# Kernel optimization log

Hardware: AMD Instinct MI355X
Metric: run time of the kernel (lower is better)

The kernel has to match this reference:

```python
import jax, jax.numpy as jnp
import numpy as np

SEQ_LEN = 12          # seq_length
K = 8                 # nsamples = 2 * num_samples
RADII = (4.0 + 1e-06, 8.0 + 1e-06, 12.0 + 1e-06)
COUT = (64, 128, 256)


def _group(xyz, s_xyz, radius):
    # ball query via knn + radius mask: xyz (B,N,3) queries, s_xyz (B,M,3) keys
    d2 = jnp.sum((xyz[:, :, None, :] - s_xyz[:, None, :, :]) ** 2, axis=-1)  # (B,N,M)
    neg, idx = jax.lax.top_k(-d2, K)                                          # (B,N,K)
    valid = (-neg) <= radius * radius
    # points outside the ball are replaced by the nearest neighbor (pad-with-first)
    return jnp.where(valid, idx, idx[..., :1])


def _gather(a, idx):
    # a (B,M,C), idx (B,N,K) -> (B,N,K,C)
    return jax.vmap(lambda t, i: t[i])(a, idx)


def _cell(xyz, feat, state, W, b, radius, cout):
    # PointRNN cell: group state points around current points, fuse
    # [displacement, current feature, state feature] with a shared linear,
    # then max-pool over the K neighbors. New state xyz = current xyz.
    B, N, _ = xyz.shape
    if state is None:
        s_xyz, s_feat = xyz, jnp.zeros((B, N, cout), xyz.dtype)
    else:
        s_xyz, s_feat = state
    idx = _group(xyz, s_xyz, radius)
    n_xyz = _gather(s_xyz, idx)                      # (B,N,K,3)
    n_feat = _gather(s_feat, idx)                    # (B,N,K,cout)
    disp = n_xyz - xyz[:, :, None, :]
    parts = [disp]
    if feat is not None:
        cin = feat.shape[-1]
        parts.append(jnp.broadcast_to(feat[:, :, None, :], (B, N, K, cin)))
    parts.append(n_feat)
    h = jnp.concatenate(parts, axis=-1) @ W + b      # (B,N,K,cout)
    return (xyz, jnp.max(h, axis=2))                 # (xyz, (B,N,cout))


def _forward(frames, W1, b1, W2, b2, W3, b3, Wm, bm, Wl, bl):
    half = SEQ_LEN // 2
    s1 = s2 = s3 = None
    # encode
    for i in range(half):
        s1 = _cell(frames[:, i], None, s1, W1, b1, RADII[0], COUT[0])
        s2 = _cell(s1[0], s1[1], s2, W2, b2, RADII[1], COUT[1])
        s3 = _cell(s2[0], s2[1], s3, W3, b3, RADII[2], COUT[2])
    # decode
    input_frame = frames[:, half - 1]
    preds = []
    for i in range(half, SEQ_LEN):
        s1 = _cell(input_frame, None, s1, W1, b1, RADII[0], COUT[0])
        s2 = _cell(s1[0], s1[1], s2, W2, b2, RADII[1], COUT[1])
        s3 = _cell(s2[0], s2[1], s3, W3, b3, RADII[2], COUT[2])
        h = jax.nn.relu(s3[1] @ Wm + bm)             # MLP([256,64]) = Lin+ReLU
        motion = h @ Wl + bl                         # (B,N,3)
        input_frame = input_frame + motion
        preds.append(input_frame)
    return jnp.stack(preds, axis=1)                  # (B, T/2, N, 3)


def setup_inputs() -> dict:
    key = jax.random.key(0)
    ks = jax.random.split(key, 12)
    B, N = 16, 512
    frames = jax.random.normal(ks[0], (B, SEQ_LEN, N, 3), jnp.float32) * 2.0

    def lin(k, fin, fout):
        k1, k2 = jax.random.split(k)
        s = 1.0 / np.sqrt(fin)
        return (jax.random.uniform(k1, (fin, fout), jnp.float32, -s, s),
                jax.random.uniform(k2, (fout,), jnp.float32, -s, s))

    W1, b1 = lin(ks[1], 3 + 0 + 64, 64)
    W2, b2 = lin(ks[2], 3 + 64 + 128, 128)
    W3, b3 = lin(ks[3], 3 + 128 + 256, 256)
    Wm, bm = lin(ks[4], 256, 64)
    Wl, bl = lin(ks[5], 64, 3)
    return {"frames": frames, "W1": W1, "b1": b1, "W2": W2, "b2": b2,
            "W3": W3, "b3": b3, "Wm": Wm, "bm": bm, "Wl": Wl, "bl": bl}


def reference(frames, W1, b1, W2, b2, W3, b3, Wm, bm, Wl, bl):
    return _forward(frames, W1, b1, W2, b2, W3, b3, Wm, bm, Wl, bl)
```

## Files before the change

kernel.cpp:

```cpp
#include <hip/hip_runtime.h>
#include <math.h>

#define BB 16
#define NN 512
#define KNN 8
#define SEQ 12
#define TQ 8
#define QB 32
#define PB 16

typedef __attribute__((ext_vector_type(8))) short bf8_t;
typedef __attribute__((ext_vector_type(4))) float f4_t;

__device__ __forceinline__ ushort f2b(float x) {
    uint u = __float_as_uint(x);
    return (ushort)((u + 0x7fffu + ((u >> 16) & 1u)) >> 16);
}
__device__ __forceinline__ float b2f(ushort h) {
    return __uint_as_float((uint)h << 16);
}
__device__ __forceinline__ void cvt8(const float* __restrict__ p,
                                     bf8_t& h, bf8_t& l) {
    float4 x0 = *(const float4*)p;
    float4 x1 = *(const float4*)(p + 4);
    float v[8] = {x0.x, x0.y, x0.z, x0.w, x1.x, x1.y, x1.z, x1.w};
#pragma unroll
    for (int i = 0; i < 8; ++i) {
        ushort hh = f2b(v[i]);
        h[i] = (short)hh;
        l[i] = (short)f2b(v[i] - b2f(hh));
    }
}

__device__ __forceinline__ void knn_body(
        const float* __restrict__ xqp, int xq_bs,
        const float* __restrict__ xsp, int xs_bs,
        int* __restrict__ idx1, int* __restrict__ idx2, int* __restrict__ idx3,
        float r2a, float r2b, float r2c,
        int ntile, int b, float* __restrict__ sm) {
    float* s   = sm;
    float* cdp = sm + 1544;
    int*   cip = (int*)(sm + 1544 + 2304);
    const int tid = threadIdx.x;

    for (int j = tid; j < NN; j += 256) {
        const float* p = xsp + (long)b * xs_bs + j * 3;
        int o = 3 * j + (j >> 6);
        s[o + 0] = p[0]; s[o + 1] = p[1]; s[o + 2] = p[2];
    }
    __syncthreads();

    int qi  = tid / TQ;
    int sub = tid % TQ;
    int n = ntile * QB + qi;
    const float* q = xqp + (long)b * xq_bs + n * 3;
    float qx = q[0], qy = q[1], qz2 = q[2];

    float bd[KNN];
    int   bi[KNN];
#pragma unroll
    for (int k = 0; k < KNN; ++k) { bd[k] = 1e30f; bi[k] = 0; }

    int j0 = sub * (NN / TQ);
    int sbase = 3 * j0 + sub;
#pragma unroll 4
    for (int jj = 0; jj < NN / TQ; ++jj) {
        float dx = s[sbase + 3 * jj + 0] - qx;
        float dy = s[sbase + 3 * jj + 1] - qy;
        float dz = s[sbase + 3 * jj + 2] - qz2;
        float d2 = fmaf(dx, dx, fmaf(dy, dy, dz * dz));
        if (d2 < bd[KNN - 1]) {
            bd[KNN - 1] = d2; bi[KNN - 1] = j0 + jj;
#pragma unroll
            for (int k = KNN - 1; k >= 1; --k) {
                if (bd[k] < bd[k - 1]) {
                    float td = bd[k]; bd[k] = bd[k - 1]; bd[k - 1] = td;
                    int   ti = bi[k]; bi[k] = bi[k - 1]; bi[k - 1] = ti;
                }
            }
        }
    }

    float* cdq = cdp + (qi * TQ + sub) * (KNN + 1);
    int*   ciq = cip + (qi * TQ + sub) * (KNN + 1);
#pragma unroll
    for (int k = 0; k < KNN; ++k) { cdq[k] = bd[k]; ciq[k] = bi[k]; }
    cdq[KNN] = 1e30f; ciq[KNN] = 0x7fffffff;
    __syncthreads();

    for (int stride = TQ / 2; stride >= 1; stride >>= 1) {
        if (sub < stride) {
            float* ca = cdp + (qi * TQ + sub) * (KNN + 1);
            float* cb = cdp + (qi * TQ + sub + stride) * (KNN + 1);
            int*   ja_p = cip + (qi * TQ + sub) * (KNN + 1);
            int*   jb_p = cip + (qi * TQ + sub + stride) * (KNN + 1);
            float rd[KNN]; int ri[KNN];
            int ia = 0, ib = 0;
#pragma unroll
            for (int k = 0; k < KNN; ++k) {
                float da = ca[ia], db = cb[ib];
                int   ja = ja_p[ia], jb = jb_p[ib];
                bool ta = (da < db) || (da == db && ja < jb);
                rd[k] = ta ? da : db; ri[k] = ta ? ja : jb;
                ia += ta ? 1 : 0; ib += ta ? 0 : 1;
            }
#pragma unroll
            for (int k = 0; k < KNN; ++k) { ca[k] = rd[k]; ja_p[k] = ri[k]; }
        }
        __syncthreads();
    }

    if (sub == 0) {
        long base = ((long)(b * NN + n)) * KNN;
        float* c0  = cdp + qi * TQ * (KNN + 1);
        int*   j0p = cip + qi * TQ * (KNN + 1);
        int i0 = j0p[0];
#pragma unroll
        for (int k = 0; k < KNN; ++k) {
            float d = c0[k]; int j = j0p[k];
            idx1[base + k] = (d <= r2a) ? j : i0;
            idx2[base + k] = (d <= r2b) ? j : i0;
            idx3[base + k] = (d <= r2c) ? j : i0;
        }
    }
}

__global__ __launch_bounds__(256) void init_kernel(
        const float* __restrict__ frames, int FB,
        int* __restrict__ i1, int* __restrict__ i2, int* __restrict__ i3,
        float r2a, float r2b, float r2c,
        const float* __restrict__ W1, const float* __restrict__ W2,
        const float* __restrict__ W3, const float* __restrict__ Wm,
        ushort* __restrict__ w1h, ushort* __restrict__ w1l,
        ushort* __restrict__ w2h, ushort* __restrict__ w2l,
        ushort* __restrict__ w3h, ushort* __restrict__ w3l,
        ushort* __restrict__ w2fh, ushort* __restrict__ w2fl,
        ushort* __restrict__ w3fh, ushort* __restrict__ w3fl,
        ushort* __restrict__ wmh, ushort* __restrict__ wml) {
    __shared__ float sm[1544 + 2304 + 2304];
    int bx = blockIdx.x;
    if (bx < 256) {
        int xcd = bx & 7, slot = bx >> 3;
        int b = xcd * 2 + (slot & 1), ntile = slot >> 1;
        knn_body(frames, FB, frames, FB, i1, i2, i3, r2a, r2b, r2c,
                 ntile, b, sm);
        return;
    }
    int t = (bx - 256) * 256 + threadIdx.x;
    float v; ushort* ph; ushort* pl; int idx;
    if (t < 4096)        { int n = t >> 6, k = t & 63;
        v = W1[(3 + k) * 64 + n];   ph = w1h;  pl = w1l;  idx = t; }
    else if (t < 20480)  { int u = t - 4096, n = u >> 7, k = u & 127;
        v = W2[(67 + k) * 128 + n]; ph = w2h;  pl = w2l;  idx = u; }
    else if (t < 86016)  { int u = t - 20480, n = u >> 8, k = u & 255;
        v = W3[(131 + k) * 256 + n]; ph = w3h; pl = w3l;  idx = u; }
    else if (t < 94208)  { int u = t - 86016, n = u >> 6, k = u & 63;
        v = W2[(3 + k) * 128 + n];  ph = w2fh; pl = w2fl; idx = u; }
    else if (t < 126976) { int u = t - 94208, n = u >> 7, k = u & 127;
        v = W3[(3 + k) * 256 + n];  ph = w3fh; pl = w3fl; idx = u; }
    else if (t < 143360) { int u = t - 126976, n = u >> 8, k = u & 255;
        v = Wm[k * 64 + n];         ph = wmh;  pl = wml;  idx = u; }
    else return;
    ushort h = f2b(v);
    ph[idx] = h; pl[idx] = f2b(v - b2f(h));
}

template<bool FIRST>
__global__ __launch_bounds__(512, 4) void cells_kernel(
        const float* __restrict__ xq, int xq_bs,
        const float* __restrict__ xs, int xs_bs,
        const int* __restrict__ i1, const int* __restrict__ i2,
        const int* __restrict__ i3,
        const float* __restrict__ G1p, const float* __restrict__ G2p,
        const float* __restrict__ G3p,
        ushort* __restrict__ s1h, ushort* __restrict__ s1l,
        ushort* __restrict__ s2h, ushort* __restrict__ s2l,
        ushort* __restrict__ s3h, ushort* __restrict__ s3l,
        const float* __restrict__ W1, const float* __restrict__ b1,
        const float* __restrict__ W2, const float* __restrict__ b2,
        const float* __restrict__ W3, const float* __restrict__ b3,
        const ushort* __restrict__ w2fh, const ushort* __restrict__ w2fl,
        const ushort* __restrict__ w3fh, const ushort* __restrict__ w3fl,
        const ushort* __restrict__ wmh, const ushort* __restrict__ wml,
        const float* __restrict__ bm,
        const float* __restrict__ Wl, const float* __restrict__ bl,
        float* __restrict__ xnext, int xn_bs, int do_head) {
    __shared__ float s1s[PB][68];
    __shared__ float s2s[PB][132];
    __shared__ float s3b[PB][260];
    __shared__ float hs[PB][64];
    __shared__ float dsp[3][PB][KNN][3];
    __shared__ int   jss[3][PB][KNN];

    const int tid = threadIdx.x;
    const int blk = blockIdx.x;
    const int xcd = blk & 7, slot = blk >> 3;
    const int b   = xcd * 2 + (slot >> 5);
    const int n0  = (slot & 31) << 4;
    const long row0 = (long)b * NN + n0;
    const long bN = (long)b * NN;
    const int wv = tid >> 6, lane = tid & 63;
    const int fm = lane & 15, quad = lane >> 4;

    for (int t = tid; t < 3 * PB * KNN; t += 512) {
        int r = t >> 7, rem = t & 127, p = rem >> 3, k = rem & 7;
        const int* ix = (r == 0) ? i1 : ((r == 1) ? i2 : i3);
        int j = ix[(row0 + p) * KNN + k];
        jss[r][p][k] = j;
        const float* sp = xs + (long)b * xs_bs + j * 3;
        const float* qp = xq + (long)b * xq_bs + (n0 + p) * 3;
        dsp[r][p][k][0] = sp[0] - qp[0];
        dsp[r][p][k][1] = sp[1] - qp[1];
        dsp[r][p][k][2] = sp[2] - qp[2];
    }
    __syncthreads();

    {
        int co = tid & 63, q = tid >> 6;
        float g1r[2][KNN];
        if (!FIRST) {
#pragma unroll
            for (int r = 0; r < 2; ++r)
#pragma unroll
                for (int k = 0; k < KNN; ++k)
                    g1r[r][k] = G1p[(bN + jss[0][2 * q + r][k]) * 64 + co];
        }
        float wx = W1[co], wy = W1[64 + co], wz = W1[128 + co];
        float bz = b1[co];
#pragma unroll
        for (int r = 0; r < 2; ++r) {
            int p = 2 * q + r;
            float acc = -1e30f;
#pragma unroll
            for (int k = 0; k < KNN; ++k) {
                float v = fmaf(dsp[0][p][k][0], wx, bz);
                v = fmaf(dsp[0][p][k][1], wy, v);
                v = fmaf(dsp[0][p][k][2], wz, v);
                if (!FIRST) v += g1r[r][k];
                acc = fmaxf(acc, v);
            }
            s1s[p][co] = acc;
            ushort h = f2b(acc);
            s1h[(row0 + p) * 64 + co] = h;
            s1l[(row0 + p) * 64 + co] = f2b(acc - b2f(h));
        }
    }
    __syncthreads();

    float4 g2r[KNN];
    {
        int c4 = tid & 31, g = tid >> 5;
        if (!FIRST) {
#pragma unroll
            for (int k = 0; k < KNN; ++k)
                g2r[k] = ((const float4*)G2p)[(bN + jss[1][g][k]) * 32 + c4];
        }
    }

    {
        int col = wv * 16 + fm;
        float bz = b2[col];
        f4_t acc = {bz, bz, bz, bz};
#pragma unroll
        for (int k0 = 0; k0 < 64; k0 += 32) {
            bf8_t ah, al; cvt8(&s1s[fm][k0 + quad * 8], ah, al);
            bf8_t bh = *(const bf8_t*)(w2fh + col * 64 + k0 + quad * 8);
            bf8_t bl = *(const bf8_t*)(w2fl + col * 64 + k0 + quad * 8);
            acc = __builtin_amdgcn_mfma_f32_16x16x32_bf16(ah, bh, acc, 0, 0, 0);
            acc = __builtin_amdgcn_mfma_f32_16x16x32_bf16(ah, bl, acc, 0, 0, 0);
            acc = __builtin_amdgcn_mfma_f32_16x16x32_bf16(al, bh, acc, 0, 0, 0);
        }
#pragma unroll
        for (int r = 0; r < 4; ++r) s2s[quad * 4 + r][col] = acc[r];
    }
    __syncthreads();

    {
        int c4 = tid & 31, g = tid >> 5;
        float4 bse = *(float4*)&s2s[g][c4 * 4];
        float4 wx = ((const float4*)W2)[c4];
        float4 wy = ((const float4*)(W2 + 128))[c4];
        float4 wz = ((const float4*)(W2 + 256))[c4];
        float4 m = make_float4(-1e30f, -1e30f, -1e30f, -1e30f);
#pragma unroll
        for (int k = 0; k < KNN; ++k) {
            float dx = dsp[1][g][k][0], dy = dsp[1][g][k][1], dz = dsp[1][g][k][2];
            float4 v;
            v.x = fmaf(dz, wz.x, fmaf(dy, wy.x, fmaf(dx, wx.x, bse.x)));
            v.y = fmaf(dz, wz.y, fmaf(dy, wy.y, fmaf(dx, wx.y, bse.y)));
            v.z = fmaf(dz, wz.z, fmaf(dy, wy.z, fmaf(dx, wx.z, bse.z)));
            v.w = fmaf(dz, wz.w, fmaf(dy, wy.w, fmaf(dx, wx.w, bse.w)));
            if (!FIRST) {
                v.x += g2r[k].x; v.y += g2r[k].y;
                v.z += g2r[k].z; v.w += g2r[k].w;
            }
            m.x = fmaxf(m.x, v.x); m.y = fmaxf(m.y, v.y);
            m.z = fmaxf(m.z, v.z); m.w = fmaxf(m.w, v.w);
        }
        *(float4*)&s2s[g][c4 * 4] = m;
        ushort4 mh, ml;
        mh.x = f2b(m.x); ml.x = f2b(m.x - b2f(mh.x));
        mh.y = f2b(m.y); ml.y = f2b(m.y - b2f(mh.y));
        mh.z = f2b(m.z); ml.z = f2b(m.z - b2f(mh.z));
        mh.w = f2b(m.w); ml.w = f2b(m.w - b2f(mh.w));
        *(ushort4*)&s2h[(row0 + g) * 128 + c4 * 4] = mh;
        *(ushort4*)&s2l[(row0 + g) * 128 + c4 * 4] = ml;
    }
    __syncthreads();

    float4 g3r[2][KNN];
    {
        int c4 = tid & 63, g = tid >> 6;
        if (!FIRST) {
#pragma unroll
            for (int r = 0; r < 2; ++r)
#pragma unroll
                for (int k = 0; k < KNN; ++k)
                    g3r[r][k] = ((const float4*)G3p)[(bN + jss[2][2 * g + r][k]) * 64 + c4];
        }
    }

    {
        int col0 = wv * 16 + fm, col1 = (wv + 8) * 16 + fm;
        float bz0 = b3[col0], bz1 = b3[col1];
        f4_t a0 = {bz0, bz0, bz0, bz0};
        f4_t a1 = {bz1, bz1, bz1, bz1};
#pragma unroll
        for (int k0 = 0; k0 < 128; k0 += 32) {
            bf8_t ah, al; cvt8(&s2s[fm][k0 + quad * 8], ah, al);
            bf8_t b0h = *(const bf8_t*)(w3fh + col0 * 128 + k0 + quad * 8);
            bf8_t b0l = *(const bf8_t*)(w3fl + col0 * 128 + k0 + quad * 8);
            bf8_t b1h = *(const bf8_t*)(w3fh + col1 * 128 + k0 + quad * 8);
            bf8_t b1l = *(const bf8_t*)(w3fl + col1 * 128 + k0 + quad * 8);
            a0 = __builtin_amdgcn_mfma_f32_16x16x32_bf16(ah, b0h, a0, 0, 0, 0);
            a0 = __builtin_amdgcn_mfma_f32_16x16x32_bf16(ah, b0l, a0, 0, 0, 0);
            a0 = __builtin_amdgcn_mfma_f32_16x16x32_bf16(al, b0h, a0, 0, 0, 0);
            a1 = __builtin_amdgcn_mfma_f32_16x16x32_bf16(ah, b1h, a1, 0, 0, 0);
            a1 = __builtin_amdgcn_mfma_f32_16x16x32_bf16(ah, b1l, a1, 0, 0, 0);
            a1 = __builtin_amdgcn_mfma_f32_16x16x32_bf16(al, b1h, a1, 0, 0, 0);
        }
#pragma unroll
        for (int r = 0; r < 4; ++r) {
            s3b[quad * 4 + r][col0] = a0[r];
            s3b[quad * 4 + r][col1] = a1[r];
        }
    }
    __syncthreads();

    {
        int c4 = tid & 63, g = tid >> 6;
        float4 wx = ((const float4*)W3)[c4];
        float4 wy = ((const float4*)(W3 + 256))[c4];
        float4 wz = ((const float4*)(W3 + 512))[c4];
#pragma unroll
        for (int r = 0; r < 2; ++r) {
            int p = 2 * g + r;
            float4 bse = *(float4*)&s3b[p][c4 * 4];
            float4 m = make_float4(-1e30f, -1e30f, -1e30f, -1e30f);
#pragma unroll
            for (int k = 0; k < KNN; ++k) {
                float dx = dsp[2][p][k][0], dy = dsp[2][p][k][1], dz = dsp[2][p][k][2];
                float4 v;
                v.x = fmaf(dz, wz.x, fmaf(dy, wy.x, fmaf(dx, wx.x, bse.x)));
                v.y = fmaf(dz, wz.y, fmaf(dy, wy.y, fmaf(dx, wx.y, bse.y)));
                v.z = fmaf(dz, wz.z, fmaf(dy, wy.z, fmaf(dx, wx.z, bse.z)));
                v.w = fmaf(dz, wz.w, fmaf(dy, wy.w, fmaf(dx, wx.w, bse.w)));
                if (!FIRST) {
                    v.x += g3r[r][k].x; v.y += g3r[r][k].y;
                    v.z += g3r[r][k].z; v.w += g3r[r][k].w;
                }
                m.x = fmaxf(m.x, v.x); m.y = fmaxf(m.y, v.y);
                m.z = fmaxf(m.z, v.z); m.w = fmaxf(m.w, v.w);
            }
            *(float4*)&s3b[p][c4 * 4] = m;
            ushort4 mh, ml;
            mh.x = f2b(m.x); ml.x = f2b(m.x - b2f(mh.x));
            mh.y = f2b(m.y); ml.y = f2b(m.y - b2f(mh.y));
            mh.z = f2b(m.z); ml.z = f2b(m.z - b2f(mh.z));
            mh.w = f2b(m.w); ml.w = f2b(m.w - b2f(mh.w));
            *(ushort4*)&s3h[(row0 + p) * 256 + c4 * 4] = mh;
            *(ushort4*)&s3l[(row0 + p) * 256 + c4 * 4] = ml;
        }
    }

    if (do_head) {
        __syncthreads();
        if (wv < 4) {
            int col = wv * 16 + fm;
            float bz = bm[col];
            f4_t acc = {bz, bz, bz, bz};
#pragma unroll
            for (int k0 = 0; k0 < 256; k0 += 32) {
                bf8_t ah, al; cvt8(&s3b[fm][k0 + quad * 8], ah, al);
                bf8_t bh = *(const bf8_t*)(wmh + col * 256 + k0 + quad * 8);
                bf8_t bl = *(const bf8_t*)(wml + col * 256 + k0 + quad * 8);
                acc = __builtin_amdgcn_mfma_f32_16x16x32_bf16(ah, bh, acc, 0, 0, 0);
                acc = __builtin_amdgcn_mfma_f32_16x16x32_bf16(ah, bl, acc, 0, 0, 0);
                acc = __builtin_amdgcn_mfma_f32_16x16x32_bf16(al, bh, acc, 0, 0, 0);
            }
#pragma unroll
            for (int r = 0; r < 4; ++r)
                hs[quad * 4 + r][col] = fmaxf(acc[r], 0.f);
        }
        __syncthreads();
        if (tid < PB * 3) {
            int p = tid / 3, d = tid % 3;
            float m = bl[d];
#pragma unroll 4
            for (int c = 0; c < 64; ++c)
                m = fmaf(hs[p][c], Wl[c * 3 + d], m);
            const float* qp = xq + (long)b * xq_bs + (n0 + p) * 3;
            xnext[(long)b * xn_bs + (n0 + p) * 3 + d] = qp[d] + m;
        }
    }
}

template<int N>
__device__ __forceinline__ void gemmTile(
        const ushort* __restrict__ Ah, const ushort* __restrict__ Al,
        const ushort* __restrict__ Bh, const ushort* __restrict__ Bl,
        float* __restrict__ G, int rb, int cb, int tid, ushort* lds) {
    const int row0 = rb * 128, c0 = cb * 64;
    ushort* ah = lds;
    ushort* al = lds + 128 * 40;
    ushort* bh = lds + 256 * 40;
    ushort* bl = lds + 320 * 40;
    const int wv = tid >> 6, lane = tid & 63;
    const int m = lane & 15, quad = lane >> 4;
    const int wm0 = wv * 32;
    const int lr = tid >> 2, ls = (tid & 3) * 8;

    f4_t acc[2][4];
#pragma unroll
    for (int rt = 0; rt < 2; ++rt)
#pragma unroll
        for (int ct = 0; ct < 4; ++ct) acc[rt][ct] = (f4_t){0.f, 0.f, 0.f, 0.f};

    bf8_t pah0, pah1, pal0, pal1, pbh, pbl;
    pah0 = *(const bf8_t*)(Ah + (long)(row0 + lr) * N + ls);
    pah1 = *(const bf8_t*)(Ah + (long)(row0 + 64 + lr) * N + ls);
    pal0 = *(const bf8_t*)(Al + (long)(row0 + lr) * N + ls);
    pal1 = *(const bf8_t*)(Al + (long)(row0 + 64 + lr) * N + ls);
    pbh  = *(const bf8_t*)(Bh + (long)(c0 + lr) * N + ls);
    pbl  = *(const bf8_t*)(Bl + (long)(c0 + lr) * N + ls);

    for (int k0 = 0; k0 < N; k0 += 32) {
        if (k0) __syncthreads();
        *(bf8_t*)(ah + lr * 40 + ls) = pah0;
        *(bf8_t*)(ah + (64 + lr) * 40 + ls) = pah1;
        *(bf8_t*)(al + lr * 40 + ls) = pal0;
        *(bf8_t*)(al + (64 + lr) * 40 + ls) = pal1;
        *(bf8_t*)(bh + lr * 40 + ls) = pbh;
        *(bf8_t*)(bl + lr * 40 + ls) = pbl;
        __syncthreads();
        if (k0 + 32 < N) {
            int kn = k0 + 32;
            pah0 = *(const bf8_t*)(Ah + (long)(row0 + lr) * N + kn + ls);
            pah1 = *(const bf8_t*)(Ah + (long)(row0 + 64 + lr) * N + kn + ls);
            pal0 = *(const bf8_t*)(Al + (long)(row0 + lr) * N + kn + ls);
            pal1 = *(const bf8_t*)(Al + (long)(row0 + 64 + lr) * N + kn + ls);
            pbh  = *(const bf8_t*)(Bh + (long)(c0 + lr) * N + kn + ls);
            pbl  = *(const bf8_t*)(Bl + (long)(c0 + lr) * N + kn + ls);
        }
        bf8_t a0h = *(const bf8_t*)(ah + (wm0 + m) * 40 + quad * 8);
        bf8_t a0l = *(const bf8_t*)(al + (wm0 + m) * 40 + quad * 8);
        bf8_t a1h = *(const bf8_t*)(ah + (wm0 + 16 + m) * 40 + quad * 8);
        bf8_t a1l = *(const bf8_t*)(al + (wm0 + 16 + m) * 40 + quad * 8);
#pragma unroll
        for (int ct = 0; ct < 4; ++ct) {
            bf8_t bth = *(const bf8_t*)(bh + (ct * 16 + m) * 40 + quad * 8);
            bf8_t btl = *(const bf8_t*)(bl + (ct * 16 + m) * 40 + quad * 8);
            acc[0][ct] = __builtin_amdgcn_mfma_f32_16x16x32_bf16(a0h, bth, acc[0][ct], 0, 0, 0);
            acc[0][ct] = __builtin_amdgcn_mfma_f32_16x16x32_bf16(a0h, btl, acc[0][ct], 0, 0, 0);
            acc[0][ct] = __builtin_amdgcn_mfma_f32_16x16x32_bf16(a0l, bth, acc[0][ct], 0, 0, 0);
            acc[1][ct] = __builtin_amdgcn_mfma_f32_16x16x32_bf16(a1h, bth, acc[1][ct], 0, 0, 0);
            acc[1][ct] = __builtin_amdgcn_mfma_f32_16x16x32_bf16(a1h, btl, acc[1][ct], 0, 0, 0);
            acc[1][ct] = __builtin_amdgcn_mfma_f32_16x16x32_bf16(a1l, bth, acc[1][ct], 0, 0, 0);
        }
    }
#pragma unroll
    for (int rt = 0; rt < 2; ++rt)
#pragma unroll
        for (int ct = 0; ct < 4; ++ct) {
            int col = c0 + ct * 16 + m;
#pragma unroll
            for (int r = 0; r < 4; ++r)
                G[(long)(row0 + wm0 + rt * 16 + quad * 4 + r) * N + col] = acc[rt][ct][r];
        }
}

__global__ __launch_bounds__(256) void gemmG_kernel(
        const ushort* __restrict__ s1h, const ushort* __restrict__ s1l,
        const ushort* __restrict__ s2h, const ushort* __restrict__ s2l,
        const ushort* __restrict__ s3h, const ushort* __restrict__ s3l,
        const ushort* __restrict__ w1h, const ushort* __restrict__ w1l,
        const ushort* __restrict__ w2h, const ushort* __restrict__ w2l,
        const ushort* __restrict__ w3h, const ushort* __restrict__ w3l,
        float* __restrict__ G1, float* __restrict__ G2,
        float* __restrict__ G3,
        const float* __restrict__ kq, int kq_bs,
        const float* __restrict__ ks, int ks_bs,
        int* __restrict__ ki1, int* __restrict__ ki2, int* __restrict__ ki3,
        float r2a, float r2b, float r2c) {
    __shared__ ushort lds[384 * 40];
    int bx = blockIdx.x, tid = threadIdx.x;
    if (bx < 256) {
        int xcd = bx & 7, slot = bx >> 3;
        int b = xcd * 2 + (slot & 1), ntile = slot >> 1;
        knn_body(kq, kq_bs, ks, ks_bs, ki1, ki2, ki3, r2a, r2b, r2c,
                 ntile, b, (float*)lds);
        return;
    }
    bx -= 256;
    if (bx < 256) {
        int xcd = bx & 7, rem = bx >> 3;
        int rb = xcd * 8 + (rem & 7), cb = rem >> 3;
        gemmTile<256>(s3h, s3l, w3h, w3l, G3, rb, cb, tid, lds);
    } else if (bx < 384) {
        int u = bx - 256; int xcd = u & 7, rem = u >> 3;
        int rb = xcd * 8 + (rem & 7), cb = rem >> 3;
        gemmTile<128>(s2h, s2l, w2h, w2l, G2, rb, cb, tid, lds);
    } else {
        int u = bx - 384; int xcd = u & 7, j = u >> 3;
        gemmTile<64>(s1h, s1l, w1h, w1l, G1, xcd * 8 + j, 0, tid, lds);
    }
}

extern "C" void kernel_launch(void* const* d_in, const int* in_sizes, int n_in,
                              void* d_out, int out_size, void* d_ws, size_t ws_size,
                              hipStream_t stream) {
    const float* frames = (const float*)d_in[0];
    const float* W1 = (const float*)d_in[1]; const float* b1 = (const float*)d_in[2];
    const float* W2 = (const float*)d_in[3]; const float* b2 = (const float*)d_in[4];
    const float* W3 = (const float*)d_in[5]; const float* b3 = (const float*)d_in[6];
    const float* Wm = (const float*)d_in[7]; const float* bm = (const float*)d_in[8];
    const float* Wl = (const float*)d_in[9]; const float* bl = (const float*)d_in[10];
    float* out = (float*)d_out;

    const long M = (long)BB * NN;
    float* ws = (float*)d_ws;
    float* G1b = ws; ws += M * 64;
    float* G2b = ws; ws += M * 128;
    float* G3b = ws; ws += M * 256;
    ushort* us = (ushort*)ws;
    ushort* s1h = us; us += M * 64;   ushort* s1l = us; us += M * 64;
    ushort* s2h = us; us += M * 128;  ushort* s2l = us; us += M * 128;
    ushort* s3h = us; us += M * 256;  ushort* s3l = us; us += M * 256;
    ushort* w1h = us; us += 4096;     ushort* w1l = us; us += 4096;
    ushort* w2h = us; us += 16384;    ushort* w2l = us; us += 16384;
    ushort* w3h = us; us += 65536;    ushort* w3l = us; us += 65536;
    ushort* w2fh = us; us += 8192;    ushort* w2fl = us; us += 8192;
    ushort* w3fh = us; us += 32768;   ushort* w3fl = us; us += 32768;
    ushort* wmh = us; us += 16384;    ushort* wml = us; us += 16384;
    const long BNK = M * KNN;
    int* ip = (int*)us;
    int* idx1w = ip; ip += 7 * BNK;
    int* idx2w = ip; ip += 7 * BNK;
    int* idx3w = ip; ip += 7 * BNK;

    double ra = 4.0 + 1e-6, rbd = 8.0 + 1e-6, rc = 12.0 + 1e-6;
    float r2a = (float)(ra * ra), r2b = (float)(rbd * rbd), r2c = (float)(rc * rc);

    const int FB = SEQ * NN * 3;
    const int OB = 6 * NN * 3;

    init_kernel<<<816, 256, 0, stream>>>(
        frames, FB, idx1w, idx2w, idx3w, r2a, r2b, r2c,
        W1, W2, W3, Wm,
        w1h, w1l, w2h, w2l, w3h, w3l,
        w2fh, w2fl, w3fh, w3fl, wmh, wml);

    for (int t = 0; t < SEQ; ++t) {
        const float* xq; int xq_bs;
        const float* xs; int xs_bs;
        if (t < 6)       { xq = frames + (long)t * NN * 3;        xq_bs = FB; }
        else if (t == 6) { xq = frames + 5L * NN * 3;             xq_bs = FB; }
        else             { xq = out + (long)(t - 7) * NN * 3;     xq_bs = OB; }
        if (t == 0)      { xs = xq;                               xs_bs = xq_bs; }
        else if (t <= 6) { xs = frames + (long)(t - 1) * NN * 3;  xs_bs = FB; }
        else if (t == 7) { xs = frames + 5L * NN * 3;             xs_bs = FB; }
        else             { xs = out + (long)(t - 8) * NN * 3;     xs_bs = OB; }

        int slot = (t <= 6) ? t : 0;
        int* i1 = idx1w + (long)slot * BNK;
        int* i2 = idx2w + (long)slot * BNK;
        int* i3 = idx3w + (long)slot * BNK;

        int do_head = (t >= 6);
        float* xnext = do_head ? out + (long)(t - 6) * NN * 3 : nullptr;

        if (t == 0)
            cells_kernel<true><<<BB * NN / PB, 512, 0, stream>>>(
                xq, xq_bs, xs, xs_bs, i1, i2, i3,
                G1b, G2b, G3b, s1h, s1l, s2h, s2l, s3h, s3l,
                W1, b1, W2, b2, W3, b3,
                w2fh, w2fl, w3fh, w3fl, wmh, wml, bm,
                Wl, bl, xnext, OB, do_head);
        else
            cells_kernel<false><<<BB * NN / PB, 512, 0, stream>>>(
                xq, xq_bs, xs, xs_bs, i1, i2, i3,
                G1b, G2b, G3b, s1h, s1l, s2h, s2l, s3h, s3l,
                W1, b1, W2, b2, W3, b3,
                w2fh, w2fl, w3fh, w3fl, wmh, wml, bm,
                Wl, bl, xnext, OB, do_head);

        if (t < SEQ - 1) {
            int tn = t + 1;
            const float* kq; int kq_bs; const float* ksp; int ks_bs; int kslot;
            if (tn <= 6) {
                int qz = tn < 5 ? tn : 5;
                kq = frames + (long)qz * NN * 3;        kq_bs = FB;
                ksp = frames + (long)(tn - 1) * NN * 3; ks_bs = FB;
                kslot = tn;
            } else {
                kq = out + (long)(tn - 7) * NN * 3;     kq_bs = OB;
                if (tn == 7) { ksp = frames + 5L * NN * 3;          ks_bs = FB; }
                else         { ksp = out + (long)(tn - 8) * NN * 3; ks_bs = OB; }
                kslot = 0;
            }
            gemmG_kernel<<<704, 256, 0, stream>>>(
                s1h, s1l, s2h, s2l, s3h, s3l,
                w1h, w1l, w2h, w2l, w3h, w3l,
                G1b, G2b, G3b,
                kq, kq_bs, ksp, ks_bs,
                idx1w + (long)kslot * BNK, idx2w + (long)kslot * BNK,
                idx3w + (long)kslot * BNK,
                r2a, r2b, r2c);
        }
    }
}
```

Measured before the change: 549.3 us.

## Fuse all timesteps into one persistent cooperative kernel with grid sync

Replaces the per-timestep sequence of cells and gemm/knn kernel launches with a single cooperative kernel of 512 blocks that loops over time and uses grid-wide synchronization between phases. It falls back to the multi-kernel path when cooperative launch or occupancy is insufficient. KNN and GEMM tiles are reworked for 512-thread blocks, and the cells stage now stores bf16 hi/lo splits directly in shared memory instead of converting from fp32. The aim is to remove about two dozen launch gaps, at the cost of grid-barrier overhead and a fixed block count that limits parallelism in each phase.

```diff
diff --git a/kernel.cpp b/kernel.cpp
--- a/kernel.cpp
+++ b/kernel.cpp
@@ -1,11 +1,14 @@
 #include <hip/hip_runtime.h>
+#include <hip/hip_cooperative_groups.h>
 #include <math.h>
+
+namespace cg = cooperative_groups;
 
 #define BB 16
 #define NN 512
 #define KNN 8
 #define SEQ 12
-#define TQ 8
+#define TQK 16
 #define QB 32
 #define PB 16
 
@@ -19,39 +22,47 @@
 __device__ __forceinline__ float b2f(ushort h) {
     return __uint_as_float((uint)h << 16);
 }
-__device__ __forceinline__ void cvt8(const float* __restrict__ p,
-                                     bf8_t& h, bf8_t& l) {
-    float4 x0 = *(const float4*)p;
-    float4 x1 = *(const float4*)(p + 4);
-    float v[8] = {x0.x, x0.y, x0.z, x0.w, x1.x, x1.y, x1.z, x1.w};
-#pragma unroll
-    for (int i = 0; i < 8; ++i) {
-        ushort hh = f2b(v[i]);
-        h[i] = (short)hh;
-        l[i] = (short)f2b(v[i] - b2f(hh));
-    }
-}
-
-__device__ __forceinline__ void knn_body(
+
+struct CellsSM {
+    float s2s[PB][132];
+    float s3f[PB][260];
+    float dsp[3][PB][KNN][3];
+    int   jss[3][PB][KNN];
+    union { ushort s1b[2][PB][72]; float hs[PB][64]; } u1;
+    ushort s2b[2][PB][136];
+    ushort s3c[2][PB][264];
+};
+union __align__(16) SM {
+    CellsSM c;
+    ushort  g[384 * 40];
+    float   kf[1544 + 4608 + 4608];
+};
+union __align__(16) GKSM {
+    ushort  g[384 * 40];
+    float   kf[1544 + 4608 + 4608];
+};
+
+__device__ __forceinline__ void knn512(
         const float* __restrict__ xqp, int xq_bs,
         const float* __restrict__ xsp, int xs_bs,
         int* __restrict__ idx1, int* __restrict__ idx2, int* __restrict__ idx3,
         float r2a, float r2b, float r2c,
-        int ntile, int b, float* __restrict__ sm) {
-    float* s   = sm;
-    float* cdp = sm + 1544;
-    int*   cip = (int*)(sm + 1544 + 2304);
+        int ntile, int b, float* __restrict__ smf) {
+    float* s   = smf;
+    float* cdp = smf + 1544;
+    int*   cip = (int*)(smf + 1544 + 4608);
     const int tid = threadIdx.x;
 
-    for (int j = tid; j < NN; j += 256) {
+    {
+        int j = tid;
         const float* p = xsp + (long)b * xs_bs + j * 3;
         int o = 3 * j + (j >> 6);
         s[o + 0] = p[0]; s[o + 1] = p[1]; s[o + 2] = p[2];
     }
     __syncthreads();
 
-    int qi  = tid / TQ;
-    int sub = tid % TQ;
+    int qi  = tid >> 4;
+    int sub = tid & 15;
     int n = ntile * QB + qi;
     const float* q = xqp + (long)b * xq_bs + n * 3;
     float qx = q[0], qy = q[1], qz2 = q[2];
@@ -61,10 +72,10 @@
 #pragma unroll
     for (int k = 0; k < KNN; ++k) { bd[k] = 1e30f; bi[k] = 0; }
 
-    int j0 = sub * (NN / TQ);
-    int sbase = 3 * j0 + sub;
+    int j0 = sub * (NN / TQK);
+    int sbase = 3 * j0 + (j0 >> 6);
 #pragma unroll 4
-    for (int jj = 0; jj < NN / TQ; ++jj) {
+    for (int jj = 0; jj < NN / TQK; ++jj) {
         float dx = s[sbase + 3 * jj + 0] - qx;
         float dy = s[sbase + 3 * jj + 1] - qy;
         float dz = s[sbase + 3 * jj + 2] - qz2;
@@ -81,19 +92,19 @@
         }
     }
 
-    float* cdq = cdp + (qi * TQ + sub) * (KNN + 1);
-    int*   ciq = cip + (qi * TQ + sub) * (KNN + 1);
+    float* cdq = cdp + (qi * TQK + sub) * (KNN + 1);
+    int*   ciq = cip + (qi * TQK + sub) * (KNN + 1);
 #pragma unroll
     for (int k = 0; k < KNN; ++k) { cdq[k] = bd[k]; ciq[k] = bi[k]; }
     cdq[KNN] = 1e30f; ciq[KNN] = 0x7fffffff;
     __syncthreads();
 
-    for (int stride = TQ / 2; stride >= 1; stride >>= 1) {
+    for (int stride = TQK / 2; stride >= 1; stride >>= 1) {
         if (sub < stride) {
-            float* ca = cdp + (qi * TQ + sub) * (KNN + 1);
-            float* cb = cdp + (qi * TQ + sub + stride) * (KNN + 1);
-            int*   ja_p = cip + (qi * TQ + sub) * (KNN + 1);
-            int*   jb_p = cip + (qi * TQ + sub + stride) * (KNN + 1);
+            float* ca = cdp + (qi * TQK + sub) * (KNN + 1);
+            float* cb = cdp + (qi * TQK + sub + stride) * (KNN + 1);
+            int*   ja_p = cip + (qi * TQK + sub) * (KNN + 1);
+            int*   jb_p = cip + (qi * TQK + sub + stride) * (KNN + 1);
             float rd[KNN]; int ri[KNN];
             int ia = 0, ib = 0;
 #pragma unroll
@@ -112,8 +123,8 @@
 
     if (sub == 0) {
         long base = ((long)(b * NN + n)) * KNN;
-        float* c0  = cdp + qi * TQ * (KNN + 1);
-        int*   j0p = cip + qi * TQ * (KNN + 1);
+        float* c0  = cdp + qi * TQK * (KNN + 1);
+        int*   j0p = cip + qi * TQK * (KNN + 1);
         int i0 = j0p[0];
 #pragma unroll
         for (int k = 0; k < KNN; ++k) {
@@ -125,48 +136,65 @@
     }
 }
 
-__global__ __launch_bounds__(256) void init_kernel(
-        const float* __restrict__ frames, int FB,
-        int* __restrict__ i1, int* __restrict__ i2, int* __restrict__ i3,
-        float r2a, float r2b, float r2c,
-        const float* __restrict__ W1, const float* __restrict__ W2,
-        const float* __restrict__ W3, const float* __restrict__ Wm,
-        ushort* __restrict__ w1h, ushort* __restrict__ w1l,
-        ushort* __restrict__ w2h, ushort* __restrict__ w2l,
-        ushort* __restrict__ w3h, ushort* __restrict__ w3l,
-        ushort* __restrict__ w2fh, ushort* __restrict__ w2fl,
-        ushort* __restrict__ w3fh, ushort* __restrict__ w3fl,
-        ushort* __restrict__ wmh, ushort* __restrict__ wml) {
-    __shared__ float sm[1544 + 2304 + 2304];
-    int bx = blockIdx.x;
-    if (bx < 256) {
-        int xcd = bx & 7, slot = bx >> 3;
-        int b = xcd * 2 + (slot & 1), ntile = slot >> 1;
-        knn_body(frames, FB, frames, FB, i1, i2, i3, r2a, r2b, r2c,
-                 ntile, b, sm);
-        return;
-    }
-    int t = (bx - 256) * 256 + threadIdx.x;
-    float v; ushort* ph; ushort* pl; int idx;
-    if (t < 4096)        { int n = t >> 6, k = t & 63;
-        v = W1[(3 + k) * 64 + n];   ph = w1h;  pl = w1l;  idx = t; }
-    else if (t < 20480)  { int u = t - 4096, n = u >> 7, k = u & 127;
-        v = W2[(67 + k) * 128 + n]; ph = w2h;  pl = w2l;  idx = u; }
-    else if (t < 86016)  { int u = t - 20480, n = u >> 8, k = u & 255;
-        v = W3[(131 + k) * 256 + n]; ph = w3h; pl = w3l;  idx = u; }
-    else if (t < 94208)  { int u = t - 86016, n = u >> 6, k = u & 63;
-        v = W2[(3 + k) * 128 + n];  ph = w2fh; pl = w2fl; idx = u; }
-    else if (t < 126976) { int u = t - 94208, n = u >> 7, k = u & 127;
-        v = W3[(3 + k) * 256 + n];  ph = w3fh; pl = w3fl; idx = u; }
-    else if (t < 143360) { int u = t - 126976, n = u >> 8, k = u & 255;
-        v = Wm[k * 64 + n];         ph = wmh;  pl = wml;  idx = u; }
-    else return;
-    ushort h = f2b(v);
-    ph[idx] = h; pl[idx] = f2b(v - b2f(h));
-}
-
-template<bool FIRST>
-__global__ __launch_bounds__(512, 4) void cells_kernel(
+template<int N>
+__device__ __forceinline__ void gemmTile512(
+        const ushort* __restrict__ Ah, const ushort* __restrict__ Al,
+        const ushort* __restrict__ Bh, const ushort* __restrict__ Bl,
+        float* __restrict__ G, int rb, int cb, int tid, ushort* lds) {
+    const int row0 = rb * 128, c0 = cb * 64;
+    ushort* ah = lds;
+    ushort* al = lds + 128 * 40;
+    ushort* bh = lds + 256 * 40;
+    ushort* bl = lds + 320 * 40;
+    const int wv = tid >> 6, lane = tid & 63;
+    const int m = lane & 15, quad = lane >> 4;
+    const int lr = tid >> 2, ls = (tid & 3) * 8;
+    const int lrB = lr & 63;
+    ushort* bstage = (tid < 256) ? bh : bl;
+    const ushort* Bsrc = (tid < 256) ? Bh : Bl;
+
+    f4_t acc[4];
+#pragma unroll
+    for (int ct = 0; ct < 4; ++ct) acc[ct] = (f4_t){0.f, 0.f, 0.f, 0.f};
+
+    bf8_t pa_h = *(const bf8_t*)(Ah + (long)(row0 + lr) * N + ls);
+    bf8_t pa_l = *(const bf8_t*)(Al + (long)(row0 + lr) * N + ls);
+    bf8_t pb   = *(const bf8_t*)(Bsrc + (long)(c0 + lrB) * N + ls);
+
+    for (int k0 = 0; k0 < N; k0 += 32) {
+        __syncthreads();
+        *(bf8_t*)(ah + lr * 40 + ls) = pa_h;
+        *(bf8_t*)(al + lr * 40 + ls) = pa_l;
+        *(bf8_t*)(bstage + lrB * 40 + ls) = pb;
+        __syncthreads();
+        if (k0 + 32 < N) {
+            int kn = k0 + 32;
+            pa_h = *(const bf8_t*)(Ah + (long)(row0 + lr) * N + kn + ls);
+            pa_l = *(const bf8_t*)(Al + (long)(row0 + lr) * N + kn + ls);
+            pb   = *(const bf8_t*)(Bsrc + (long)(c0 + lrB) * N + kn + ls);
+        }
+        bf8_t a_h = *(const bf8_t*)(ah + (wv * 16 + m) * 40 + quad * 8);
+        bf8_t a_l = *(const bf8_t*)(al + (wv * 16 + m) * 40 + quad * 8);
+#pragma unroll
+        for (int ct = 0; ct < 4; ++ct) {
+            bf8_t bth = *(const bf8_t*)(bh + (ct * 16 + m) * 40 + quad * 8);
+            bf8_t btl = *(const bf8_t*)(bl + (ct * 16 + m) * 40 + quad * 8);
+            acc[ct] = __builtin_amdgcn_mfma_f32_16x16x32_bf16(a_h, bth, acc[ct], 0, 0, 0);
+            acc[ct] = __builtin_amdgcn_mfma_f32_16x16x32_bf16(a_h, btl, acc[ct], 0, 0, 0);
+            acc[ct] = __builtin_amdgcn_mfma_f32_16x16x32_bf16(a_l, bth, acc[ct], 0, 0, 0);
+        }
+    }
+#pragma unroll
+    for (int ct = 0; ct < 4; ++ct) {
+        int col = c0 + ct * 16 + m;
+#pragma unroll
+        for (int r = 0; r < 4; ++r)
+            G[(long)(row0 + wv * 16 + quad * 4 + r) * N + col] = acc[ct][r];
+    }
+}
+
+__device__ __forceinline__ void cells_phase(
+        bool first,
         const float* __restrict__ xq, int xq_bs,
         const float* __restrict__ xs, int xs_bs,
         const int* __restrict__ i1, const int* __restrict__ i2,
@@ -184,16 +212,8 @@
         const ushort* __restrict__ wmh, const ushort* __restrict__ wml,
         const float* __restrict__ bm,
         const float* __restrict__ Wl, const float* __restrict__ bl,
-        float* __restrict__ xnext, int xn_bs, int do_head) {
-    __shared__ float s1s[PB][68];
-    __shared__ float s2s[PB][132];
-    __shared__ float s3b[PB][260];
-    __shared__ float hs[PB][64];
-    __shared__ float dsp[3][PB][KNN][3];
-    __shared__ int   jss[3][PB][KNN];
-
-    const int tid = threadIdx.x;
-    const int blk = blockIdx.x;
+        float* __restrict__ xnext, int xn_bs, int do_head,
+        int blk, int tid, CellsSM& sm) {
     const int xcd = blk & 7, slot = blk >> 3;
     const int b   = xcd * 2 + (slot >> 5);
     const int n0  = (slot & 31) << 4;
@@ -206,24 +226,24 @@
         int r = t >> 7, rem = t & 127, p = rem >> 3, k = rem & 7;
         const int* ix = (r == 0) ? i1 : ((r == 1) ? i2 : i3);
         int j = ix[(row0 + p) * KNN + k];
-        jss[r][p][k] = j;
+        sm.jss[r][p][k] = j;
         const float* sp = xs + (long)b * xs_bs + j * 3;
         const float* qp = xq + (long)b * xq_bs + (n0 + p) * 3;
-        dsp[r][p][k][0] = sp[0] - qp[0];
-        dsp[r][p][k][1] = sp[1] - qp[1];
-        dsp[r][p][k][2] = sp[2] - qp[2];
+        sm.dsp[r][p][k][0] = sp[0] - qp[0];
+        sm.dsp[r][p][k][1] = sp[1] - qp[1];
+        sm.dsp[r][p][k][2] = sp[2] - qp[2];
     }
     __syncthreads();
 
     {
         int co = tid & 63, q = tid >> 6;
         float g1r[2][KNN];
-        if (!FIRST) {
+        if (!first) {
 #pragma unroll
             for (int r = 0; r < 2; ++r)
 #pragma unroll
                 for (int k = 0; k < KNN; ++k)
-                    g1r[r][k] = G1p[(bN + jss[0][2 * q + r][k]) * 64 + co];
+                    g1r[r][k] = G1p[(bN + sm.jss[0][2 * q + r][k]) * 64 + co];
         }
         float wx = W1[co], wy = W1[64 + co], wz = W1[128 + co];
         float bz = b1[co];
@@ -233,16 +253,18 @@
             float acc = -1e30f;
 #pragma unroll
             for (int k = 0; k < KNN; ++k) {
-                float v = fmaf(dsp[0][p][k][0], wx, bz);
-                v = fmaf(dsp[0][p][k][1], wy, v);
-                v = fmaf(dsp[0][p][k][2], wz, v);
-                if (!FIRST) v += g1r[r][k];
+                float v = fmaf(sm.dsp[0][p][k][0], wx, bz);
+                v = fmaf(sm.dsp[0][p][k][1], wy, v);
+                v = fmaf(sm.dsp[0][p][k][2], wz, v);
+                if (!first) v += g1r[r][k];
                 acc = fmaxf(acc, v);
             }
-            s1s[p][co] = acc;
             ushort h = f2b(acc);
+            ushort l = f2b(acc - b2f(h));
+            sm.u1.s1b[0][p][co] = h;
+            sm.u1.s1b[1][p][co] = l;
             s1h[(row0 + p) * 64 + co] = h;
-            s1l[(row0 + p) * 64 + co] = f2b(acc - b2f(h));
+            s1l[(row0 + p) * 64 + co] = l;
         }
     }
     __syncthreads();
@@ -250,10 +272,10 @@
     float4 g2r[KNN];
     {
         int c4 = tid & 31, g = tid >> 5;
-        if (!FIRST) {
+        if (!first) {
 #pragma unroll
             for (int k = 0; k < KNN; ++k)
-                g2r[k] = ((const float4*)G2p)[(bN + jss[1][g][k]) * 32 + c4];
+                g2r[k] = ((const float4*)G2p)[(bN + sm.jss[1][g][k]) * 32 + c4];
         }
     }
 
@@ -263,7 +285,8 @@
         f4_t acc = {bz, bz, bz, bz};
 #pragma unroll
         for (int k0 = 0; k0 < 64; k0 += 32) {
-            bf8_t ah, al; cvt8(&s1s[fm][k0 + quad * 8], ah, al);
+            bf8_t ah = *(const bf8_t*)&sm.u1.s1b[0][fm][k0 + quad * 8];
+            bf8_t al = *(const bf8_t*)&sm.u1.s1b[1][fm][k0 + quad * 8];
             bf8_t bh = *(const bf8_t*)(w2fh + col * 64 + k0 + quad * 8);
             bf8_t bl = *(const bf8_t*)(w2fl + col * 64 + k0 + quad * 8);
             acc = __builtin_amdgcn_mfma_f32_16x16x32_bf16(ah, bh, acc, 0, 0, 0);
@@ -271,38 +294,40 @@
             acc = __builtin_amdgcn_mfma_f32_16x16x32_bf16(al, bh, acc, 0, 0, 0);
         }
 #pragma unroll
-        for (int r = 0; r < 4; ++r) s2s[quad * 4 + r][col] = acc[r];
+        for (int r = 0; r < 4; ++r) sm.s2s[quad * 4 + r][col] = acc[r];
     }
     __syncthreads();
 
     {
         int c4 = tid & 31, g = tid >> 5;
-        float4 bse = *(float4*)&s2s[g][c4 * 4];
+        float4 bse = *(float4*)&sm.s2s[g][c4 * 4];
         float4 wx = ((const float4*)W2)[c4];
         float4 wy = ((const float4*)(W2 + 128))[c4];
         float4 wz = ((const float4*)(W2 + 256))[c4];
         float4 m = make_float4(-1e30f, -1e30f, -1e30f, -1e30f);
 #pragma unroll
         for (int k = 0; k < KNN; ++k) {
-            float dx = dsp[1][g][k][0], dy = dsp[1][g][k][1], dz = dsp[1][g][k][2];
+            float dx = sm.dsp[1][g][k][0], dy = sm.dsp[1][g][k][1],
+                  dz = sm.dsp[1][g][k][2];
             float4 v;
             v.x = fmaf(dz, wz.x, fmaf(dy, wy.x, fmaf(dx, wx.x, bse.x)));
             v.y = fmaf(dz, wz.y, fmaf(dy, wy.y, fmaf(dx, wx.y, bse.y)));
             v.z = fmaf(dz, wz.z, fmaf(dy, wy.z, fmaf(dx, wx.z, bse.z)));
             v.w = fmaf(dz, wz.w, fmaf(dy, wy.w, fmaf(dx, wx.w, bse.w)));
-            if (!FIRST) {
+            if (!first) {
                 v.x += g2r[k].x; v.y += g2r[k].y;
                 v.z += g2r[k].z; v.w += g2r[k].w;
             }
             m.x = fmaxf(m.x, v.x); m.y = fmaxf(m.y, v.y);
             m.z = fmaxf(m.z, v.z); m.w = fmaxf(m.w, v.w);
         }
-        *(float4*)&s2s[g][c4 * 4] = m;
         ushort4 mh, ml;
         mh.x = f2b(m.x); ml.x = f2b(m.x - b2f(mh.x));
         mh.y = f2b(m.y); ml.y = f2b(m.y - b2f(mh.y));
         mh.z = f2b(m.z); ml.z = f2b(m.z - b2f(mh.z));
         mh.w = f2b(m.w); ml.w = f2b(m.w - b2f(mh.w));
+        *(ushort4*)&sm.s2b[0][g][c4 * 4] = mh;
+        *(ushort4*)&sm.s2b[1][g][c4 * 4] = ml;
         *(ushort4*)&s2h[(row0 + g) * 128 + c4 * 4] = mh;
         *(ushort4*)&s2l[(row0 + g) * 128 + c4 * 4] = ml;
     }
@@ -311,12 +336,12 @@
     float4 g3r[2][KNN];
     {
         int c4 = tid & 63, g = tid >> 6;
-        if (!FIRST) {
+        if (!first) {
 #pragma unroll
             for (int r = 0; r < 2; ++r)
 #pragma unroll
                 for (int k = 0; k < KNN; ++k)
-                    g3r[r][k] = ((const float4*)G3p)[(bN + jss[2][2 * g + r][k]) * 64 + c4];
+                    g3r[r][k] = ((const float4*)G3p)[(bN + sm.jss[2][2 * g + r][k]) * 64 + c4];
         }
     }
 
@@ -327,7 +352,8 @@
         f4_t a1 = {bz1, bz1, bz1, bz1};
 #pragma unroll
         for (int k0 = 0; k0 < 128; k0 += 32) {
-            bf8_t ah, al; cvt8(&s2s[fm][k0 + quad * 8], ah, al);
+            bf8_t ah = *(const bf8_t*)&sm.s2b[0][fm][k0 + quad * 8];
+            bf8_t al = *(const bf8_t*)&sm.s2b[1][fm][k0 + quad * 8];
             bf8_t b0h = *(const bf8_t*)(w3fh + col0 * 128 + k0 + quad * 8);
             bf8_t b0l = *(const bf8_t*)(w3fl + col0 * 128 + k0 + quad * 8);
             bf8_t b1h = *(const bf8_t*)(w3fh + col1 * 128 + k0 + quad * 8);
@@ -341,8 +367,8 @@
         }
 #pragma unroll
         for (int r = 0; r < 4; ++r) {
-            s3b[quad * 4 + r][col0] = a0[r];
-            s3b[quad * 4 + r][col1] = a1[r];
+            sm.s3f[quad * 4 + r][col0] = a0[r];
+            sm.s3f[quad * 4 + r][col1] = a1[r];
         }
     }
     __syncthreads();
@@ -355,29 +381,31 @@
 #pragma unroll
         for (int r = 0; r < 2; ++r) {
             int p = 2 * g + r;
-            float4 bse = *(float4*)&s3b[p][c4 * 4];
+            float4 bse = *(float4*)&sm.s3f[p][c4 * 4];
             float4 m = make_float4(-1e30f, -1e30f, -1e30f, -1e30f);
 #pragma unroll
             for (int k = 0; k < KNN; ++k) {
-                float dx = dsp[2][p][k][0], dy = dsp[2][p][k][1], dz = dsp[2][p][k][2];
+                float dx = sm.dsp[2][p][k][0], dy = sm.dsp[2][p][k][1],
+                      dz = sm.dsp[2][p][k][2];
                 float4 v;
                 v.x = fmaf(dz, wz.x, fmaf(dy, wy.x, fmaf(dx, wx.x, bse.x)));
                 v.y = fmaf(dz, wz.y, fmaf(dy, wy.y, fmaf(dx, wx.y, bse.y)));
                 v.z = fmaf(dz, wz.z, fmaf(dy, wy.z, fmaf(dx, wx.z, bse.z)));
                 v.w = fmaf(dz, wz.w, fmaf(dy, wy.w, fmaf(dx, wx.w, bse.w)));
-                if (!FIRST) {
+                if (!first) {
                     v.x += g3r[r][k].x; v.y += g3r[r][k].y;
                     v.z += g3r[r][k].z; v.w += g3r[r][k].w;
                 }
                 m.x = fmaxf(m.x, v.x); m.y = fmaxf(m.y, v.y);
                 m.z = fmaxf(m.z, v.z); m.w = fmaxf(m.w, v.w);
             }
-            *(float4*)&s3b[p][c4 * 4] = m;
             ushort4 mh, ml;
             mh.x = f2b(m.x); ml.x = f2b(m.x - b2f(mh.x));
             mh.y = f2b(m.y); ml.y = f2b(m.y - b2f(mh.y));
             mh.z = f2b(m.z); ml.z = f2b(m.z - b2f(mh.z));
             mh.w = f2b(m.w); ml.w = f2b(m.w - b2f(mh.w));
+            *(ushort4*)&sm.s3c[0][p][c4 * 4] = mh;
+            *(ushort4*)&sm.s3c[1][p][c4 * 4] = ml;
             *(ushort4*)&s3h[(row0 + p) * 256 + c4 * 4] = mh;
             *(ushort4*)&s3l[(row0 + p) * 256 + c4 * 4] = ml;
         }
@@ -391,16 +419,20 @@
             f4_t acc = {bz, bz, bz, bz};
 #pragma unroll
             for (int k0 = 0; k0 < 256; k0 += 32) {
-                bf8_t ah, al; cvt8(&s3b[fm][k0 + quad * 8], ah, al);
+                bf8_t ah = *(const bf8_t*)&sm.s3c[0][fm][k0 + quad * 8];
+                bf8_t al = *(const bf8_t*)&sm.s3c[1][fm][k0 + quad * 8];
                 bf8_t bh = *(const bf8_t*)(wmh + col * 256 + k0 + quad * 8);
                 bf8_t bl = *(const bf8_t*)(wml + col * 256 + k0 + quad * 8);
                 acc = __builtin_amdgcn_mfma_f32_16x16x32_bf16(ah, bh, acc, 0, 0, 0);
                 acc = __builtin_amdgcn_mfma_f32_16x16x32_bf16(ah, bl, acc, 0, 0, 0);
                 acc = __builtin_amdgcn_mfma_f32_16x16x32_bf16(al, bh, acc, 0, 0, 0);
             }
+            __syncthreads();
 #pragma unroll
             for (int r = 0; r < 4; ++r)
-                hs[quad * 4 + r][col] = fmaxf(acc[r], 0.f);
+                sm.u1.hs[quad * 4 + r][col] = fmaxf(acc[r], 0.f);
+        } else {
+            __syncthreads();
         }
         __syncthreads();
         if (tid < PB * 3) {
@@ -408,121 +440,216 @@
             float m = bl[d];
 #pragma unroll 4
             for (int c = 0; c < 64; ++c)
-                m = fmaf(hs[p][c], Wl[c * 3 + d], m);
+                m = fmaf(sm.u1.hs[p][c], Wl[c * 3 + d], m);
             const float* qp = xq + (long)b * xq_bs + (n0 + p) * 3;
             xnext[(long)b * xn_bs + (n0 + p) * 3 + d] = qp[d] + m;
         }
     }
 }
 
-template<int N>
-__device__ __forceinline__ void gemmTile(
-        const ushort* __restrict__ Ah, const ushort* __restrict__ Al,
-        const ushort* __restrict__ Bh, const ushort* __restrict__ Bl,
-        float* __restrict__ G, int rb, int cb, int tid, ushort* lds) {
-    const int row0 = rb * 128, c0 = cb * 64;
-    ushort* ah = lds;
-    ushort* al = lds + 128 * 40;
-    ushort* bh = lds + 256 * 40;
-    ushort* bl = lds + 320 * 40;
-    const int wv = tid >> 6, lane = tid & 63;
-    const int m = lane & 15, quad = lane >> 4;
-    const int wm0 = wv * 32;
-    const int lr = tid >> 2, ls = (tid & 3) * 8;
-
-    f4_t acc[2][4];
-#pragma unroll
-    for (int rt = 0; rt < 2; ++rt)
-#pragma unroll
-        for (int ct = 0; ct < 4; ++ct) acc[rt][ct] = (f4_t){0.f, 0.f, 0.f, 0.f};
-
-    bf8_t pah0, pah1, pal0, pal1, pbh, pbl;
-    pah0 = *(const bf8_t*)(Ah + (long)(row0 + lr) * N + ls);
-    pah1 = *(const bf8_t*)(Ah + (long)(row0 + 64 + lr) * N + ls);
-    pal0 = *(const bf8_t*)(Al + (long)(row0 + lr) * N + ls);
-    pal1 = *(const bf8_t*)(Al + (long)(row0 + 64 + lr) * N + ls);
-    pbh  = *(const bf8_t*)(Bh + (long)(c0 + lr) * N + ls);
-    pbl  = *(const bf8_t*)(Bl + (long)(c0 + lr) * N + ls);
-
-    for (int k0 = 0; k0 < N; k0 += 32) {
-        if (k0) __syncthreads();
-        *(bf8_t*)(ah + lr * 40 + ls) = pah0;
-        *(bf8_t*)(ah + (64 + lr) * 40 + ls) = pah1;
-        *(bf8_t*)(al + lr * 40 + ls) = pal0;
-        *(bf8_t*)(al + (64 + lr) * 40 + ls) = pal1;
-        *(bf8_t*)(bh + lr * 40 + ls) = pbh;
-        *(bf8_t*)(bl + lr * 40 + ls) = pbl;
-        __syncthreads();
-        if (k0 + 32 < N) {
-            int kn = k0 + 32;
-            pah0 = *(const bf8_t*)(Ah + (long)(row0 + lr) * N + kn + ls);
-            pah1 = *(const bf8_t*)(Ah + (long)(row0 + 64 + lr) * N + kn + ls);
-            pal0 = *(const bf8_t*)(Al + (long)(row0 + lr) * N + kn + ls);
-            pal1 = *(const bf8_t*)(Al + (long)(row0 + 64 + lr) * N + kn + ls);
-            pbh  = *(const bf8_t*)(Bh + (long)(c0 + lr) * N + kn + ls);
-            pbl  = *(const bf8_t*)(Bl + (long)(c0 + lr) * N + kn + ls);
-        }
-        bf8_t a0h = *(const bf8_t*)(ah + (wm0 + m) * 40 + quad * 8);
-        bf8_t a0l = *(const bf8_t*)(al + (wm0 + m) * 40 + quad * 8);
-        bf8_t a1h = *(const bf8_t*)(ah + (wm0 + 16 + m) * 40 + quad * 8);
-        bf8_t a1l = *(const bf8_t*)(al + (wm0 + 16 + m) * 40 + quad * 8);
-#pragma unroll
-        for (int ct = 0; ct < 4; ++ct) {
-            bf8_t bth = *(const bf8_t*)(bh + (ct * 16 + m) * 40 + quad * 8);
-            bf8_t btl = *(const bf8_t*)(bl + (ct * 16 + m) * 40 + quad * 8);
-            acc[0][ct] = __builtin_amdgcn_mfma_f32_16x16x32_bf16(a0h, bth, acc[0][ct], 0, 0, 0);
-            acc[0][ct] = __builtin_amdgcn_mfma_f32_16x16x32_bf16(a0h, btl, acc[0][ct], 0, 0, 0);
-            acc[0][ct] = __builtin_amdgcn_mfma_f32_16x16x32_bf16(a0l, bth, acc[0][ct], 0, 0, 0);
-            acc[1][ct] = __builtin_amdgcn_mfma_f32_16x16x32_bf16(a1h, bth, acc[1][ct], 0, 0, 0);
-            acc[1][ct] = __builtin_amdgcn_mfma_f32_16x16x32_bf16(a1h, btl, acc[1][ct], 0, 0, 0);
-            acc[1][ct] = __builtin_amdgcn_mfma_f32_16x16x32_bf16(a1l, bth, acc[1][ct], 0, 0, 0);
-        }
-    }
-#pragma unroll
-    for (int rt = 0; rt < 2; ++rt)
-#pragma unroll
-        for (int ct = 0; ct < 4; ++ct) {
-            int col = c0 + ct * 16 + m;
-#pragma unroll
-            for (int r = 0; r < 4; ++r)
-                G[(long)(row0 + wm0 + rt * 16 + quad * 4 + r) * N + col] = acc[rt][ct][r];
-        }
-}
-
-__global__ __launch_bounds__(256) void gemmG_kernel(
-        const ushort* __restrict__ s1h, const ushort* __restrict__ s1l,
-        const ushort* __restrict__ s2h, const ushort* __restrict__ s2l,
-        const ushort* __restrict__ s3h, const ushort* __restrict__ s3l,
-        const ushort* __restrict__ w1h, const ushort* __restrict__ w1l,
-        const ushort* __restrict__ w2h, const ushort* __restrict__ w2l,
-        const ushort* __restrict__ w3h, const ushort* __restrict__ w3l,
-        float* __restrict__ G1, float* __restrict__ G2,
-        float* __restrict__ G3,
+__device__ __forceinline__ void convW_one(int id,
+        const float* __restrict__ W1, const float* __restrict__ W2,
+        const float* __restrict__ W3, const float* __restrict__ Wm,
+        ushort* w1h, ushort* w1l, ushort* w2h, ushort* w2l,
+        ushort* w3h, ushort* w3l, ushort* w2fh, ushort* w2fl,
+        ushort* w3fh, ushort* w3fl, ushort* wmh, ushort* wml) {
+    float v; ushort* ph; ushort* pl; int idx;
+    if (id < 4096)        { int n = id >> 6, k = id & 63;
+        v = W1[(3 + k) * 64 + n];   ph = w1h;  pl = w1l;  idx = id; }
+    else if (id < 20480)  { int u = id - 4096, n = u >> 7, k = u & 127;
+        v = W2[(67 + k) * 128 + n]; ph = w2h;  pl = w2l;  idx = u; }
+    else if (id < 86016)  { int u = id - 20480, n = u >> 8, k = u & 255;
+        v = W3[(131 + k) * 256 + n]; ph = w3h; pl = w3l;  idx = u; }
+    else if (id < 94208)  { int u = id - 86016, n = u >> 6, k = u & 63;
+        v = W2[(3 + k) * 128 + n];  ph = w2fh; pl = w2fl; idx = u; }
+    else if (id < 126976) { int u = id - 94208, n = u >> 7, k = u & 127;
+        v = W3[(3 + k) * 256 + n];  ph = w3fh; pl = w3fl; idx = u; }
+    else if (id < 143360) { int u = id - 126976, n = u >> 8, k = u & 255;
+        v = Wm[k * 64 + n];         ph = wmh;  pl = wml;  idx = u; }
+    else return;
+    ushort h = f2b(v);
+    ph[idx] = h; pl[idx] = f2b(v - b2f(h));
+}
+
+__global__ __launch_bounds__(512, 4) void fused_kernel(
+        const float* frames, float* out,
+        float* G1, float* G2, float* G3,
+        ushort* s1h, ushort* s1l, ushort* s2h, ushort* s2l,
+        ushort* s3h, ushort* s3l,
+        ushort* w1h, ushort* w1l, ushort* w2h, ushort* w2l,
+        ushort* w3h, ushort* w3l,
+        ushort* w2fh, ushort* w2fl, ushort* w3fh, ushort* w3fl,
+        ushort* wmh, ushort* wml,
+        int* idx1w, int* idx2w, int* idx3w,
+        const float* W1, const float* b1, const float* W2, const float* b2,
+        const float* W3, const float* b3, const float* Wm, const float* bm,
+        const float* Wl, const float* bl,
+        float r2a, float r2b, float r2c) {
+    __shared__ SM sm;
+    cg::grid_group grid = cg::this_grid();
+    const int bx = blockIdx.x, tid = threadIdx.x;
+    const int FB = SEQ * NN * 3, OB = 6 * NN * 3;
+    const long BNK = (long)BB * NN * KNN;
+
+    convW_one(bx * 512 + tid, W1, W2, W3, Wm,
+              w1h, w1l, w2h, w2l, w3h, w3l,
+              w2fh, w2fl, w3fh, w3fl, wmh, wml);
+    if (bx < 256) {
+        int xcd = bx & 7, slot = bx >> 3;
+        int b = xcd * 2 + (slot & 1), ntile = slot >> 1;
+        knn512(frames, FB, frames, FB, idx1w, idx2w, idx3w,
+               r2a, r2b, r2c, ntile, b, sm.kf);
+    }
+    __threadfence(); grid.sync(); __threadfence();
+
+    for (int t = 0; t < SEQ; ++t) {
+        const float* xq; int xq_bs; const float* xs; int xs_bs;
+        if (t < 6)       { xq = frames + (long)t * NN * 3;        xq_bs = FB; }
+        else if (t == 6) { xq = frames + 5L * NN * 3;             xq_bs = FB; }
+        else             { xq = out + (long)(t - 7) * NN * 3;     xq_bs = OB; }
+        if (t == 0)      { xs = xq;                               xs_bs = xq_bs; }
+        else if (t <= 6) { xs = frames + (long)(t - 1) * NN * 3;  xs_bs = FB; }
+        else if (t == 7) { xs = frames + 5L * NN * 3;             xs_bs = FB; }
+        else             { xs = out + (long)(t - 8) * NN * 3;     xs_bs = OB; }
+        int slot = (t <= 6) ? t : 0;
+        const int* i1 = idx1w + slot * BNK;
+        const int* i2 = idx2w + slot * BNK;
+        const int* i3 = idx3w + slot * BNK;
+        int do_head = (t >= 6);
+        float* xnext = do_head ? out + (long)(t - 6) * NN * 3 : nullptr;
+
+        cells_phase(t == 0, xq, xq_bs, xs, xs_bs, i1, i2, i3,
+                    G1, G2, G3, s1h, s1l, s2h, s2l, s3h, s3l,
+                    W1, b1, W2, b2, W3, b3,
+                    w2fh, w2fl, w3fh, w3fl, wmh, wml, bm,
+                    Wl, bl, xnext, OB, do_head, bx, tid, sm.c);
+
+        if (t == SEQ - 1) break;
+        __threadfence(); grid.sync(); __threadfence();
+
+        if (bx < 256) {
+            int tn = t + 1;
+            const float* kq; int kq_bs; const float* ksp; int ks_bs; int kslot;
+            if (tn <= 6) {
+                int qz = tn < 5 ? tn : 5;
+                kq = frames + (long)qz * NN * 3;        kq_bs = FB;
+                ksp = frames + (long)(tn - 1) * NN * 3; ks_bs = FB;
+                kslot = tn;
+            } else {
+                kq = out + (long)(tn - 7) * NN * 3;     kq_bs = OB;
+                if (tn == 7) { ksp = frames + 5L * NN * 3;          ks_bs = FB; }
+                else         { ksp = out + (long)(tn - 8) * NN * 3; ks_bs = OB; }
+                kslot = 0;
+            }
+            int xcd = bx & 7, slot2 = bx >> 3;
+            int b = xcd * 2 + (slot2 & 1), ntile = slot2 >> 1;
+            knn512(kq, kq_bs, ksp, ks_bs,
+                   idx1w + (long)kslot * BNK, idx2w + (long)kslot * BNK,
+                   idx3w + (long)kslot * BNK,
+                   r2a, r2b, r2c, ntile, b, sm.kf);
+        } else {
+            for (int it = bx - 256; it < 448; it += 256) {
+                if (it < 256) {
+                    int xcd = it & 7, rem = it >> 3;
+                    int rb = xcd * 8 + (rem & 7), cb = rem >> 3;
+                    gemmTile512<256>(s3h, s3l, w3h, w3l, G3, rb, cb, tid, sm.g);
+                } else if (it < 384) {
+                    int u = it - 256; int xcd = u & 7, rem = u >> 3;
+                    int rb = xcd * 8 + (rem & 7), cb = rem >> 3;
+                    gemmTile512<128>(s2h, s2l, w2h, w2l, G2, rb, cb, tid, sm.g);
+                } else {
+                    int u = it - 384; int xcd = u & 7, j = u >> 3;
+                    gemmTile512<64>(s1h, s1l, w1h, w1l, G1, xcd * 8 + j, 0, tid, sm.g);
+                }
+            }
+        }
+        __threadfence(); grid.sync(); __threadfence();
+    }
+}
+
+__global__ __launch_bounds__(512) void init512_kernel(
+        const float* __restrict__ frames, int FB,
+        int* __restrict__ i1, int* __restrict__ i2, int* __restrict__ i3,
+        float r2a, float r2b, float r2c,
+        const float* __restrict__ W1, const float* __restrict__ W2,
+        const float* __restrict__ W3, const float* __restrict__ Wm,
+        ushort* w1h, ushort* w1l, ushort* w2h, ushort* w2l,
+        ushort* w3h, ushort* w3l, ushort* w2fh, ushort* w2fl,
+        ushort* w3fh, ushort* w3fl, ushort* wmh, ushort* wml) {
+    __shared__ float kf[1544 + 4608 + 4608];
+    int bx = blockIdx.x;
+    if (bx < 256) {
+        int xcd = bx & 7, slot = bx >> 3;
+        int b = xcd * 2 + (slot & 1), ntile = slot >> 1;
+        knn512(frames, FB, frames, FB, i1, i2, i3, r2a, r2b, r2c,
+               ntile, b, kf);
+        return;
+    }
+    convW_one((bx - 256) * 512 + threadIdx.x, W1, W2, W3, Wm,
+              w1h, w1l, w2h, w2l, w3h, w3l,
+              w2fh, w2fl, w3fh, w3fl, wmh, wml);
+}
+
+__global__ __launch_bounds__(512) void cells512_kernel(
+        int first,
+        const float* __restrict__ xq, int xq_bs,
+        const float* __restrict__ xs, int xs_bs,
+        const int* __restrict__ i1, const int* __restrict__ i2,
+        const int* __restrict__ i3,
+        const float* __restrict__ G1p, const float* __restrict__ G2p,
+        const float* __restrict__ G3p,
+        ushort* s1h, ushort* s1l, ushort* s2h, ushort* s2l,
+        ushort* s3h, ushort* s3l,
+        const float* __restrict__ W1, const float* __restrict__ b1,
+        const float* __restrict__ W2, const float* __restrict__ b2,
+        const float* __restrict__ W3, const float* __restrict__ b3,
+        const ushort* __restrict__ w2fh, const ushort* __restrict__ w2fl,
+        const ushort* __restrict__ w3fh, const ushort* __restrict__ w3fl,
+        const ushort* __restrict__ wmh, const ushort* __restrict__ wml,
+        const float* __restrict__ bm,
+        const float* __restrict__ Wl, const float* __restrict__ bl,
+        float* xnext, int xn_bs, int do_head) {
+    __shared__ CellsSM sm;
+    cells_phase(first != 0, xq, xq_bs, xs, xs_bs, i1, i2, i3,
+                G1p, G2p, G3p, s1h, s1l, s2h, s2l, s3h, s3l,
+                W1, b1, W2, b2, W3, b3, w2fh, w2fl, w3fh, w3fl,
+                wmh, wml, bm, Wl, bl, xnext, xn_bs, do_head,
+                blockIdx.x, threadIdx.x, sm);
+}
+
+__global__ __launch_bounds__(512) void gemmknn512_kernel(
+        const ushort* s1h, const ushort* s1l,
+        const ushort* s2h, const ushort* s2l,
+        const ushort* s3h, const ushort* s3l,
+        const ushort* w1h, const ushort* w1l,
+        const ushort* w2h, const ushort* w2l,
+        const ushort* w3h, const ushort* w3l,
+        float* G1, float* G2, float* G3,
         const float* __restrict__ kq, int kq_bs,
         const float* __restrict__ ks, int ks_bs,
-        int* __restrict__ ki1, int* __restrict__ ki2, int* __restrict__ ki3,
+        int* ki1, int* ki2, int* ki3,
         float r2a, float r2b, float r2c) {
-    __shared__ ushort lds[384 * 40];
+    __shared__ GKSM sm;
     int bx = blockIdx.x, tid = threadIdx.x;
     if (bx < 256) {
         int xcd = bx & 7, slot = bx >> 3;
         int b = xcd * 2 + (slot & 1), ntile = slot >> 1;
-        knn_body(kq, kq_bs, ks, ks_bs, ki1, ki2, ki3, r2a, r2b, r2c,
-                 ntile, b, (float*)lds);
+        knn512(kq, kq_bs, ks, ks_bs, ki1, ki2, ki3, r2a, r2b, r2c,
+               ntile, b, sm.kf);
         return;
     }
-    bx -= 256;
-    if (bx < 256) {
-        int xcd = bx & 7, rem = bx >> 3;
+    int it = bx - 256;
+    if (it < 256) {
+        int xcd = it & 7, rem = it >> 3;
         int rb = xcd * 8 + (rem & 7), cb = rem >> 3;
-        gemmTile<256>(s3h, s3l, w3h, w3l, G3, rb, cb, tid, lds);
-    } else if (bx < 384) {
-        int u = bx - 256; int xcd = u & 7, rem = u >> 3;
+        gemmTile512<256>(s3h, s3l, w3h, w3l, G3, rb, cb, tid, sm.g);
+    } else if (it < 384) {
+        int u = it - 256; int xcd = u & 7, rem = u >> 3;
         int rb = xcd * 8 + (rem & 7), cb = rem >> 3;
-        gemmTile<128>(s2h, s2l, w2h, w2l, G2, rb, cb, tid, lds);
+        gemmTile512<128>(s2h, s2l, w2h, w2l, G2, rb, cb, tid, sm.g);
     } else {
-        int u = bx - 384; int xcd = u & 7, j = u >> 3;
-        gemmTile<64>(s1h, s1l, w1h, w1l, G1, xcd * 8 + j, 0, tid, lds);
+        int u = it - 384; int xcd = u & 7, j = u >> 3;
+        gemmTile512<64>(s1h, s1l, w1h, w1l, G1, xcd * 8 + j, 0, tid, sm.g);
     }
 }
 
@@ -564,68 +691,100 @@
     const int FB = SEQ * NN * 3;
     const int OB = 6 * NN * 3;
 
-    init_kernel<<<816, 256, 0, stream>>>(
-        frames, FB, idx1w, idx2w, idx3w, r2a, r2b, r2c,
-        W1, W2, W3, Wm,
-        w1h, w1l, w2h, w2l, w3h, w3l,
-        w2fh, w2fl, w3fh, w3fl, wmh, wml);
-
-    for (int t = 0; t < SEQ; ++t) {
-        const float* xq; int xq_bs;
-        const float* xs; int xs_bs;
-        if (t < 6)       { xq = frames + (long)t * NN * 3;        xq_bs = FB; }
-        else if (t == 6) { xq = frames + 5L * NN * 3;             xq_bs = FB; }
-        else             { xq = out + (long)(t - 7) * NN * 3;     xq_bs = OB; }
-        if (t == 0)      { xs = xq;                               xs_bs = xq_bs; }
-        else if (t <= 6) { xs = frames + (long)(t - 1) * NN * 3;  xs_bs = FB; }
-        else if (t == 7) { xs = frames + 5L * NN * 3;             xs_bs = FB; }
-        else             { xs = out + (long)(t - 8) * NN * 3;     xs_bs = OB; }
-
-        int slot = (t <= 6) ? t : 0;
-        int* i1 = idx1w + (long)slot * BNK;
-        int* i2 = idx2w + (long)slot * BNK;
-        int* i3 = idx3w + (long)slot * BNK;
-
-        int do_head = (t >= 6);
-        float* xnext = do_head ? out + (long)(t - 6) * NN * 3 : nullptr;
-
-        if (t == 0)
-            cells_kernel<true><<<BB * NN / PB, 512, 0, stream>>>(
-                xq, xq_bs, xs, xs_bs, i1, i2, i3,
+    static int g_coop = -1;
+    if (g_coop < 0) {
+        int attr = 0, dev = 0, nb = 0;
+        hipGetDevice(&dev);
+        hipDeviceGetAttribute(&attr, hipDeviceAttributeCooperativeLaunch, dev);
+        hipDeviceProp_t prop{};
+        hipGetDeviceProperties(&prop, dev);
+        if (attr &&
+            hipOccupancyMaxActiveBlocksPerMultiprocessor(
+                &nb, fused_kernel, 512, 0) == hipSuccess &&
+            nb * prop.multiProcessorCount >= 512)
+            g_coop = 1;
+        else
+            g_coop = 0;
+    }
+
+    bool did_coop = false;
+    if (g_coop == 1) {
+        void* args[] = {
+            (void*)&frames, (void*)&out,
+            (void*)&G1b, (void*)&G2b, (void*)&G3b,
+            (void*)&s1h, (void*)&s1l, (void*)&s2h, (void*)&s2l,
+            (void*)&s3h, (void*)&s3l,
+            (void*)&w1h, (void*)&w1l, (void*)&w2h, (void*)&w2l,
+            (void*)&w3h, (void*)&w3l,
+            (void*)&w2fh, (void*)&w2fl, (void*)&w3fh, (void*)&w3fl,
+            (void*)&wmh, (void*)&wml,
+            (void*)&idx1w, (void*)&idx2w, (void*)&idx3w,
+            (void*)&W1, (void*)&b1, (void*)&W2, (void*)&b2,
+            (void*)&W3, (void*)&b3, (void*)&Wm, (void*)&bm,
+            (void*)&Wl, (void*)&bl,
+            (void*)&r2a, (void*)&r2b, (void*)&r2c
+        };
+        hipError_t e = hipLaunchCooperativeKernel((const void*)fused_kernel,
+                                                  dim3(512), dim3(512),
+                                                  args, 0, stream);
+        did_coop = (e == hipSuccess);
+        if (!did_coop) g_coop = 0;
+    }
+
+    if (!did_coop) {
+        init512_kernel<<<536, 512, 0, stream>>>(
+            frames, FB, idx1w, idx2w, idx3w, r2a, r2b, r2c,
+            W1, W2, W3, Wm, w1h, w1l, w2h, w2l, w3h, w3l,
+            w2fh, w2fl, w3fh, w3fl, wmh, wml);
+
+        for (int t = 0; t < SEQ; ++t) {
+            const float* xq; int xq_bs; const float* xs; int xs_bs;
+            if (t < 6)       { xq = frames + (long)t * NN * 3;        xq_bs = FB; }
+            else if (t == 6) { xq = frames + 5L * NN * 3;             xq_bs = FB; }
+            else             { xq = out + (long)(t - 7) * NN * 3;     xq_bs = OB; }
+            if (t == 0)      { xs = xq;                               xs_bs = xq_bs; }
+            else if (t <= 6) { xs = frames + (long)(t - 1) * NN * 3;  xs_bs = FB; }
+            else if (t == 7) { xs = frames + 5L * NN * 3;             xs_bs = FB; }
+            else             { xs = out + (long)(t - 8) * NN * 3;     xs_bs = OB; }
+
+            int slot = (t <= 6) ? t : 0;
+            int* i1 = idx1w + (long)slot * BNK;
+            int* i2 = idx2w + (long)slot * BNK;
+            int* i3 = idx3w + (long)slot * BNK;
+
+            int do_head = (t >= 6);
+            float* xnext = do_head ? out + (long)(t - 6) * NN * 3 : nullptr;
+
+            cells512_kernel<<<BB * NN / PB, 512, 0, stream>>>(
+                t == 0 ? 1 : 0, xq, xq_bs, xs, xs_bs, i1, i2, i3,
                 G1b, G2b, G3b, s1h, s1l, s2h, s2l, s3h, s3l,
                 W1, b1, W2, b2, W3, b3,
                 w2fh, w2fl, w3fh, w3fl, wmh, wml, bm,
                 Wl, bl, xnext, OB, do_head);
-        else
-            cells_kernel<false><<<BB * NN / PB, 512, 0, stream>>>(
-                xq, xq_bs, xs, xs_bs, i1, i2, i3,
-                G1b, G2b, G3b, s1h, s1l, s2h, s2l, s3h, s3l,
-                W1, b1, W2, b2, W3, b3,
-                w2fh, w2fl, w3fh, w3fl, wmh, wml, bm,
-                Wl, bl, xnext, OB, do_head);
-
-        if (t < SEQ - 1) {
-            int tn = t + 1;
-            const float* kq; int kq_bs; const float* ksp; int ks_bs; int kslot;
-            if (tn <= 6) {
-                int qz = tn < 5 ? tn : 5;
-                kq = frames + (long)qz * NN * 3;        kq_bs = FB;
-                ksp = frames + (long)(tn - 1) * NN * 3; ks_bs = FB;
-                kslot = tn;
-            } else {
-                kq = out + (long)(tn - 7) * NN * 3;     kq_bs = OB;
-                if (tn == 7) { ksp = frames + 5L * NN * 3;          ks_bs = FB; }
-                else         { ksp = out + (long)(tn - 8) * NN * 3; ks_bs = OB; }
-                kslot = 0;
-            }
-            gemmG_kernel<<<704, 256, 0, stream>>>(
-                s1h, s1l, s2h, s2l, s3h, s3l,
-                w1h, w1l, w2h, w2l, w3h, w3l,
-                G1b, G2b, G3b,
-                kq, kq_bs, ksp, ks_bs,
-                idx1w + (long)kslot * BNK, idx2w + (long)kslot * BNK,
-                idx3w + (long)kslot * BNK,
-                r2a, r2b, r2c);
-        }
-    }
-}
+
+            if (t < SEQ - 1) {
+                int tn = t + 1;
+                const float* kq; int kq_bs; const float* ksp; int ks_bs; int kslot;
+                if (tn <= 6) {
+                    int qz = tn < 5 ? tn : 5;
+                    kq = frames + (long)qz * NN * 3;        kq_bs = FB;
+                    ksp = frames + (long)(tn - 1) * NN * 3; ks_bs = FB;
+                    kslot = tn;
+                } else {
+                    kq = out + (long)(tn - 7) * NN * 3;     kq_bs = OB;
+                    if (tn == 7) { ksp = frames + 5L * NN * 3;          ks_bs = FB; }
+                    else         { ksp = out + (long)(tn - 8) * NN * 3; ks_bs = OB; }
+                    kslot = 0;
+                }
+                gemmknn512_kernel<<<704, 512, 0, stream>>>(
+                    s1h, s1l, s2h, s2l, s3h, s3l,
+                    w1h, w1l, w2h, w2l, w3h, w3l,
+                    G1b, G2b, G3b,
+                    kq, kq_bs, ksp, ks_bs,
+                    idx1w + (long)kslot * BNK, idx2w + (long)kslot * BNK,
+                    idx3w + (long)kslot * BNK,
+                    r2a, r2b, r2c);
+            }
+        }
+    }
+}
```

Result: faster. 531.8 us (-3.2%).
